# Kernel tuning notes

Hardware: AMD Instinct MI355X
Metric: run time of the kernel (lower is better)

Reference implementation:

```python
import jax, jax.numpy as jnp
import numpy as np

D_MODEL = 512
N_PAIRS = D_MODEL // 2
B, T = 8, 4096


def setup_inputs() -> dict:
    key = jax.random.key(0)
    ks = jax.random.split(key, 7)
    scale = 1.0 / np.sqrt(D_MODEL)
    return {
        "x_seq": jax.random.normal(ks[0], (B, T, D_MODEL), dtype=jnp.float32),
        "W_angle": jax.random.uniform(ks[1], (D_MODEL, N_PAIRS), jnp.float32, -scale, scale),
        "b_angle": jnp.zeros((N_PAIRS,), jnp.float32),
        "W_decay": jax.random.uniform(ks[2], (D_MODEL, 1), jnp.float32, -scale, scale),
        "b_decay": jnp.full((1,), 1.4, jnp.float32),
        "W_input": jax.random.uniform(ks[3], (D_MODEL, D_MODEL), jnp.float32, -scale, scale),
        "b_input": jax.random.uniform(ks[4], (D_MODEL,), jnp.float32, -scale, scale),
    }


def _givens_ssm(x_seq, W_angle, b_angle, W_decay, b_decay, W_input, b_input):
    Bb, Tt, D = x_seq.shape
    P = D // 2
    angles = jnp.einsum("btd,dp->btp", x_seq, W_angle) + b_angle          # [B,T,P]
    decays = jax.nn.sigmoid(jnp.einsum("btd,dk->btk", x_seq, W_decay) + b_decay)[..., 0]  # [B,T]
    inj = jnp.einsum("btd,de->bte", x_seq, W_input) + b_input              # [B,T,D]
    inj = inj.reshape(Bb, Tt, P, 2)

    # scan over time: h_t = decay_t * Rot(angles_t) h_{t-1} + inj_t, pairwise 2x2 rotations
    def step(h, inp):
        a, d, u = inp  # a:[B,P], d:[B], u:[B,P,2]
        c, s = jnp.cos(a), jnp.sin(a)
        he = c * h[..., 0] - s * h[..., 1]
        ho = s * h[..., 0] + c * h[..., 1]
        h_new = d[:, None, None] * jnp.stack([he, ho], axis=-1) + u
        return h_new, h_new

    h0 = jnp.zeros((Bb, P, 2), x_seq.dtype)
    xs = (jnp.swapaxes(angles, 0, 1), jnp.swapaxes(decays, 0, 1), jnp.swapaxes(inj, 0, 1))
    _, states = jax.lax.scan(step, h0, xs)  # [T,B,P,2]
    return jnp.swapaxes(states, 0, 1).reshape(Bb, Tt, D)


def reference(x_seq, W_angle, b_angle, W_decay, b_decay, W_input, b_input):
    return _givens_ssm(x_seq, W_angle, b_angle, W_decay, b_decay, W_input, b_input)
```

## Files before the change

### kernel.cpp

```cpp
#include <hip/hip_runtime.h>
#include <math.h>

typedef _Float16 half_t;
typedef __attribute__((ext_vector_type(8))) _Float16 half8;
typedef __attribute__((ext_vector_type(4))) _Float16 half4;
typedef __attribute__((ext_vector_type(2))) _Float16 half2v;
typedef __attribute__((ext_vector_type(4))) float floatx4;

#define BATCH   8
#define SEQ     4096
#define DM      512
#define NP      256
#define M_TOT   32768
#define NTOT    768
#define CHUNKS  512
#define CHUNK_LEN 8

__device__ __forceinline__ void async_load16(const void* g, void* l) {
    __builtin_amdgcn_global_load_lds((const __attribute__((address_space(1))) void*)g,
                                     (__attribute__((address_space(3))) void*)l,
                                     16, 0, 0);
}

__global__ __launch_bounds__(256) void decay_convert(const float* __restrict__ X,
                                                     const float* __restrict__ Wd,
                                                     const float* __restrict__ bd,
                                                     float* __restrict__ dec,
                                                     half_t* __restrict__ Xh) {
    const int wave = threadIdx.x >> 6;
    const int lane = threadIdx.x & 63;
    const int row0 = blockIdx.x * 8 + wave * 2;
    const float4* x0 = (const float4*)(X + (size_t)row0 * DM);
    const float4* x1 = x0 + 128;
    const float4* wd = (const float4*)Wd;
    float4 a0 = x0[2 * lane], a1 = x0[2 * lane + 1];
    float4 b0 = x1[2 * lane], b1 = x1[2 * lane + 1];
    float4 w0 = wd[2 * lane], w1 = wd[2 * lane + 1];
    float s0 = a0.x * w0.x + a0.y * w0.y + a0.z * w0.z + a0.w * w0.w
             + a1.x * w1.x + a1.y * w1.y + a1.z * w1.z + a1.w * w1.w;
    float s1 = b0.x * w0.x + b0.y * w0.y + b0.z * w0.z + b0.w * w0.w
             + b1.x * w1.x + b1.y * w1.y + b1.z * w1.z + b1.w * w1.w;
    half8 h0 = {(half_t)a0.x, (half_t)a0.y, (half_t)a0.z, (half_t)a0.w,
                (half_t)a1.x, (half_t)a1.y, (half_t)a1.z, (half_t)a1.w};
    half8 h1 = {(half_t)b0.x, (half_t)b0.y, (half_t)b0.z, (half_t)b0.w,
                (half_t)b1.x, (half_t)b1.y, (half_t)b1.z, (half_t)b1.w};
    *(half8*)(Xh + (size_t)row0 * DM + lane * 8) = h0;
    *(half8*)(Xh + (size_t)(row0 + 1) * DM + lane * 8) = h1;
#pragma unroll
    for (int off = 32; off > 0; off >>= 1) {
        s0 += __shfl_down(s0, off, 64);
        s1 += __shfl_down(s1, off, 64);
    }
    if (lane == 0) {
        dec[row0]     = 1.0f / (1.0f + __expf(-(s0 + bd[0])));
        dec[row0 + 1] = 1.0f / (1.0f + __expf(-(s1 + bd[0])));
    }
}

__global__ __launch_bounds__(256) void wcat_transpose(const float* __restrict__ Wi,
                                                      const float* __restrict__ Wa,
                                                      half_t* __restrict__ Wt) {
    const int idx = blockIdx.x * 256 + threadIdx.x;
    const int n = idx >> 9;
    const int k = idx & 511;
    float v = (n < DM) ? Wi[(size_t)k * DM + n] : Wa[(size_t)k * NP + (n - DM)];
    Wt[idx] = (half_t)v;
}

__global__ __launch_bounds__(256) void gemm_fused(const half_t* __restrict__ Xh,
                                                  const half_t* __restrict__ Wt,
                                                  const float* __restrict__ bi,
                                                  const float* __restrict__ ba,
                                                  half_t* __restrict__ inj,
                                                  half_t* __restrict__ angles) {
    __shared__ __align__(16) char As[8192];
    __shared__ __align__(16) char Bs[8192];

    const int bm   = blockIdx.x;
    const int bn   = blockIdx.y;
    const int tid  = threadIdx.x;
    const int wave = tid >> 6;
    const int lane = tid & 63;
    const int quad = lane >> 4;
    const int l16  = lane & 15;
    const int wrow = wave >> 1;
    const int wcol = wave & 1;

    floatx4 acc[4][4];
#pragma unroll
    for (int i = 0; i < 4; ++i)
#pragma unroll
        for (int j = 0; j < 4; ++j) acc[i][j] = (floatx4){0.f, 0.f, 0.f, 0.f};

    const int s0 = wave * 128 + lane;
    const int s1 = s0 + 64;
    const int r0 = s0 >> 2, kql0 = (s0 & 3) ^ ((r0 >> 1) & 3);
    const int r1 = s1 >> 2, kql1 = (s1 & 3) ^ ((r1 >> 1) & 3);
    const half_t* gA0 = Xh + (size_t)(bm * 128 + r0) * DM + kql0 * 8;
    const half_t* gA1 = Xh + (size_t)(bm * 128 + r1) * DM + kql1 * 8;
    const half_t* gB0 = Wt + (size_t)(bn * 128 + r0) * DM + kql0 * 8;
    const half_t* gB1 = Wt + (size_t)(bn * 128 + r1) * DM + kql1 * 8;
    char* lA0 = As + wave * 2048;
    char* lA1 = As + wave * 2048 + 1024;
    char* lB0 = Bs + wave * 2048;
    char* lB1 = Bs + wave * 2048 + 1024;

    for (int k0 = 0; k0 < DM; k0 += 32) {
        async_load16(gA0 + k0, lA0);
        async_load16(gA1 + k0, lA1);
        async_load16(gB0 + k0, lB0);
        async_load16(gB1 + k0, lB1);
        __syncthreads();

        half8 af[4], bf[4];
#pragma unroll
        for (int mt = 0; mt < 4; ++mt) {
            const int r = wrow * 64 + mt * 16 + l16;
            af[mt] = *(const half8*)(As + r * 64 + ((quad ^ ((r >> 1) & 3)) << 4));
        }
#pragma unroll
        for (int nt = 0; nt < 4; ++nt) {
            const int r = wcol * 64 + nt * 16 + l16;
            bf[nt] = *(const half8*)(Bs + r * 64 + ((quad ^ ((r >> 1) & 3)) << 4));
        }
#pragma unroll
        for (int mt = 0; mt < 4; ++mt)
#pragma unroll
            for (int nt = 0; nt < 4; ++nt)
                acc[mt][nt] = __builtin_amdgcn_mfma_f32_16x16x32_f16(af[mt], bf[nt],
                                                                     acc[mt][nt], 0, 0, 0);
        __syncthreads();
    }

    const bool  is_inj = (bn < 4);
    half_t*     dst    = is_inj ? inj    : angles;
    const int   ldd    = is_inj ? DM     : NP;
    const int   cb     = is_inj ? bn * 128 : bn * 128 - DM;

    float bias[4];
#pragma unroll
    for (int nt = 0; nt < 4; ++nt) {
        const int colt = wcol * 64 + nt * 16 + l16;
        bias[nt] = is_inj ? bi[bn * 128 + colt] : ba[bn * 128 + colt - DM];
    }

    half_t* Cs = (half_t*)As;
#pragma unroll
    for (int rh = 0; rh < 2; ++rh) {
        __syncthreads();
        if (wrow == rh) {
#pragma unroll
            for (int mt = 0; mt < 4; ++mt)
#pragma unroll
                for (int nt = 0; nt < 4; ++nt)
#pragma unroll
                    for (int r = 0; r < 4; ++r) {
                        const int lr = mt * 16 + quad * 4 + r;
                        const int lc = wcol * 64 + nt * 16 + l16;
                        Cs[lr * 128 + (lc ^ (((lr >> 2) & 3) << 4))] =
                            (half_t)(acc[mt][nt][r] + bias[nt]);
                    }
        }
        __syncthreads();
#pragma unroll
        for (int it = 0; it < 4; ++it) {
            const int idx = it * 256 + tid;
            const int rr  = idx >> 4;
            const int cc  = (idx & 15) * 8;
            const int grow = bm * 128 + rh * 64 + rr;
            half8 v = *(half8*)(Cs + rr * 128 + (cc ^ (((rr >> 2) & 3) << 4)));
            *(half8*)(dst + (size_t)grow * ldd + cb + cc) = v;
        }
    }
}

__global__ __launch_bounds__(256) void scan_sum1(const half_t* __restrict__ angles,
                                                 const float* __restrict__ decays,
                                                 const half_t* __restrict__ inj,
                                                 float* __restrict__ thetaC,
                                                 float4* __restrict__ hend,
                                                 float* __restrict__ Dprod) {
    const int b   = blockIdx.x >> 8;
    const int sub = threadIdx.x >> 7;
    const int th  = threadIdx.x & 127;
    const int c   = (blockIdx.x & 255) * 2 + sub;
    const int p0  = th * 2;
    const int t0  = c * CHUNK_LEN;

    const half_t* ap = angles + (size_t)(b * SEQ + t0) * NP + p0;
    const half4*  up = (const half4*)(inj + (size_t)(b * SEQ + t0) * DM) + th;
    const float*  dp = decays + b * SEQ + t0;

    half2v a[8]; half4 u[8]; float d[8];
#pragma unroll
    for (int j = 0; j < 8; ++j) {
        a[j] = *(const half2v*)(ap + (size_t)j * NP);
        u[j] = up[(size_t)j * 128];
        d[j] = dp[j];
    }

    float h0a = 0, h1a = 0, h0b = 0, h1b = 0, tha = 0, thb = 0, dc = 1.0f;
#pragma unroll
    for (int j = 0; j < 8; ++j) {
        float a0 = (float)a[j][0], a1 = (float)a[j][1];
        float dd = d[j];
        float s0, c0, s1, c1;
        __sincosf(a0, &s0, &c0);
        __sincosf(a1, &s1, &c1);
        float n0a = fmaf(dd, c0 * h0a - s0 * h1a, (float)u[j][0]);
        float n1a = fmaf(dd, s0 * h0a + c0 * h1a, (float)u[j][1]);
        float n0b = fmaf(dd, c1 * h0b - s1 * h1b, (float)u[j][2]);
        float n1b = fmaf(dd, s1 * h0b + c1 * h1b, (float)u[j][3]);
        h0a = n0a; h1a = n1a; h0b = n0b; h1b = n1b;
        tha += a0; thb += a1; dc *= dd;
    }
    const size_t cbase = (size_t)(b * CHUNKS + c) * NP + p0;
    *(float2*)(thetaC + cbase) = make_float2(tha, thb);
    hend[cbase >> 1] = make_float4(h0a, h1a, h0b, h1b);
    if (th == 0) Dprod[b * CHUNKS + c] = dc;
}

__global__ __launch_bounds__(512) void scan_chunks(const float* __restrict__ thetaC,
                                                   const float4* __restrict__ hend,
                                                   const float* __restrict__ Dprod,
                                                   float4* __restrict__ hentry) {
    const int b  = blockIdx.x >> 7;
    const int pp = blockIdx.x & 127;
    const int c  = threadIdx.x;

    __shared__ float  sTa[512], sTb[512], sD[512];
    __shared__ float4 sV[512];

    const size_t idx = (size_t)(b * CHUNKS + c);
    const float2 th2 = *(const float2*)(thetaC + idx * NP + pp * 2);
    float4 v = hend[idx * 128 + pp];
    float  D = Dprod[idx];
    float tha = th2.x, thb = th2.y;

    sTa[c] = tha; sTb[c] = thb; sD[c] = D; sV[c] = v;

#pragma unroll
    for (int o = 1; o < 512; o <<= 1) {
        __syncthreads();
        float lta = 0.f, ltb = 0.f, lD = 0.f;
        float4 lv = make_float4(0.f, 0.f, 0.f, 0.f);
        const bool has = (c >= o);
        if (has) { lta = sTa[c - o]; ltb = sTb[c - o]; lD = sD[c - o]; lv = sV[c - o]; }
        __syncthreads();
        if (has) {
            float s0, c0, s1, c1;
            __sincosf(tha, &s0, &c0);
            __sincosf(thb, &s1, &c1);
            v.x = fmaf(D, c0 * lv.x - s0 * lv.y, v.x);
            v.y = fmaf(D, s0 * lv.x + c0 * lv.y, v.y);
            v.z = fmaf(D, c1 * lv.z - s1 * lv.w, v.z);
            v.w = fmaf(D, s1 * lv.z + c1 * lv.w, v.w);
            tha += lta; thb += ltb; D *= lD;
            sTa[c] = tha; sTb[c] = thb; sD[c] = D; sV[c] = v;
        }
    }
    __syncthreads();
    const float4 e = (c == 0) ? make_float4(0.f, 0.f, 0.f, 0.f) : sV[c - 1];
    hentry[idx * 128 + pp] = e;
}

__global__ __launch_bounds__(256) void scan_final(const half_t* __restrict__ angles,
                                                  const float* __restrict__ decays,
                                                  const half_t* __restrict__ inj,
                                                  const float4* __restrict__ hentry,
                                                  float* __restrict__ out) {
    const int b   = blockIdx.x >> 8;
    const int sub = threadIdx.x >> 7;
    const int th  = threadIdx.x & 127;
    const int c   = (blockIdx.x & 255) * 2 + sub;
    const int p0  = th * 2;
    const int t0  = c * CHUNK_LEN;

    const half_t* ap = angles + (size_t)(b * SEQ + t0) * NP + p0;
    const half4*  up = (const half4*)(inj + (size_t)(b * SEQ + t0) * DM) + th;
    float4*       op = (float4*)out + (size_t)(b * SEQ + t0) * 128 + (p0 >> 1);
    const float*  dp = decays + b * SEQ + t0;

    float4 v = hentry[(size_t)(b * CHUNKS + c) * 128 + (p0 >> 1)];
    float h0a = v.x, h1a = v.y, h0b = v.z, h1b = v.w;

    half2v a[8]; half4 u[8]; float d[8];
#pragma unroll
    for (int j = 0; j < 8; ++j) {
        a[j] = *(const half2v*)(ap + (size_t)j * NP);
        u[j] = up[(size_t)j * 128];
        d[j] = dp[j];
    }

#pragma unroll
    for (int j = 0; j < 8; ++j) {
        float a0 = (float)a[j][0], a1 = (float)a[j][1];
        float dd = d[j];
        float s0, c0, s1, c1;
        __sincosf(a0, &s0, &c0);
        __sincosf(a1, &s1, &c1);
        float n0a = fmaf(dd, c0 * h0a - s0 * h1a, (float)u[j][0]);
        float n1a = fmaf(dd, s0 * h0a + c0 * h1a, (float)u[j][1]);
        float n0b = fmaf(dd, c1 * h0b - s1 * h1b, (float)u[j][2]);
        float n1b = fmaf(dd, s1 * h0b + c1 * h1b, (float)u[j][3]);
        h0a = n0a; h1a = n1a; h0b = n0b; h1b = n1b;
        op[(size_t)j * 128] = make_float4(h0a, h1a, h0b, h1b);
    }
}

extern "C" void kernel_launch(void* const* d_in, const int* in_sizes, int n_in,
                              void* d_out, int out_size, void* d_ws, size_t ws_size,
                              hipStream_t stream) {
    const float* x  = (const float*)d_in[0];
    const float* Wa = (const float*)d_in[1];
    const float* ba = (const float*)d_in[2];
    const float* Wd = (const float*)d_in[3];
    const float* bd = (const float*)d_in[4];
    const float* Wi = (const float*)d_in[5];
    const float* bi = (const float*)d_in[6];
    float* out = (float*)d_out;

    char* ws = (char*)d_ws;
    half_t* x_h     = (half_t*)(ws);
    float*  thetaC  = (float*)(ws);
    float4* hend    = (float4*)(ws + 4194304);
    float*  Dprod   = (float*)(ws + 12582912);
    float4* hentry  = (float4*)(ws + 12599296);
    half_t* inj_h   = (half_t*)(ws + 33554432);
    half_t* angles  = (half_t*)(ws + 67108864);
    float*  decays  = (float*)(ws + 83886080);
    half_t* Wcat_t  = (half_t*)(ws + 84017152);

    decay_convert<<<M_TOT / 8, 256, 0, stream>>>(x, Wd, bd, decays, x_h);
    wcat_transpose<<<(NTOT * DM) / 256, 256, 0, stream>>>(Wi, Wa, Wcat_t);
    gemm_fused<<<dim3(M_TOT / 128, NTOT / 128), 256, 0, stream>>>(x_h, Wcat_t, bi, ba, inj_h, angles);

    scan_sum1<<<BATCH * CHUNKS / 2, 256, 0, stream>>>(angles, decays, inj_h, thetaC, hend, Dprod);
    scan_chunks<<<BATCH * 128, 512, 0, stream>>>(thetaC, hend, Dprod, hentry);
    scan_final<<<BATCH * CHUNKS / 2, 256, 0, stream>>>(angles, decays, inj_h, hentry, out);
}
```

Baseline: 214.7 us.

## Precompute cos/sin in GEMM epilogue, stage injection in output, double chunk length

The GEMM epilogue now computes sin/cos of the angles once and stores them as two fp16 planes. The injection term is written directly into the fp32 output buffer, and the final scan reads and overwrites it in place. The chunk scan carries composed rotation cos/sin pairs instead of summed angles, and chunk length doubles to 16, which halves the chunk count. This removes the repeated sincos work from both scan passes and the fp16 injection buffer. In exchange the injection is read in fp32 (more bytes), the angle data is stored twice, and the epilogue does more work.

Result: slower. 228.0 us (+6.2%).

```diff
diff --git a/kernel.cpp b/kernel.cpp
--- a/kernel.cpp
+++ b/kernel.cpp
@@ -13,8 +13,8 @@
 #define NP      256
 #define M_TOT   32768
 #define NTOT    768
-#define CHUNKS  512
-#define CHUNK_LEN 8
+#define CHUNKS  256
+#define CHUNK_LEN 16
 
 __device__ __forceinline__ void async_load16(const void* g, void* l) {
     __builtin_amdgcn_global_load_lds((const __attribute__((address_space(1))) void*)g,
@@ -71,8 +71,9 @@
                                                   const half_t* __restrict__ Wt,
                                                   const float* __restrict__ bi,
                                                   const float* __restrict__ ba,
-                                                  half_t* __restrict__ inj,
-                                                  half_t* __restrict__ angles) {
+                                                  float* __restrict__ out,
+                                                  half_t* __restrict__ cosb,
+                                                  half_t* __restrict__ sinb) {
     __shared__ __align__(16) char As[8192];
     __shared__ __align__(16) char Bs[8192];
 
@@ -132,95 +133,119 @@
         __syncthreads();
     }
 
-    const bool  is_inj = (bn < 4);
-    half_t*     dst    = is_inj ? inj    : angles;
-    const int   ldd    = is_inj ? DM     : NP;
-    const int   cb     = is_inj ? bn * 128 : bn * 128 - DM;
-
-    float bias[4];
-#pragma unroll
-    for (int nt = 0; nt < 4; ++nt) {
-        const int colt = wcol * 64 + nt * 16 + l16;
-        bias[nt] = is_inj ? bi[bn * 128 + colt] : ba[bn * 128 + colt - DM];
-    }
-
-    half_t* Cs = (half_t*)As;
-#pragma unroll
-    for (int rh = 0; rh < 2; ++rh) {
-        __syncthreads();
-        if (wrow == rh) {
-#pragma unroll
-            for (int mt = 0; mt < 4; ++mt)
-#pragma unroll
-                for (int nt = 0; nt < 4; ++nt)
-#pragma unroll
-                    for (int r = 0; r < 4; ++r) {
-                        const int lr = mt * 16 + quad * 4 + r;
-                        const int lc = wcol * 64 + nt * 16 + l16;
-                        Cs[lr * 128 + (lc ^ (((lr >> 2) & 3) << 4))] =
-                            (half_t)(acc[mt][nt][r] + bias[nt]);
-                    }
-        }
-        __syncthreads();
-#pragma unroll
-        for (int it = 0; it < 4; ++it) {
-            const int idx = it * 256 + tid;
-            const int rr  = idx >> 4;
-            const int cc  = (idx & 15) * 8;
-            const int grow = bm * 128 + rh * 64 + rr;
-            half8 v = *(half8*)(Cs + rr * 128 + (cc ^ (((rr >> 2) & 3) << 4)));
-            *(half8*)(dst + (size_t)grow * ldd + cb + cc) = v;
-        }
-    }
-}
-
-__global__ __launch_bounds__(256) void scan_sum1(const half_t* __restrict__ angles,
+    const bool is_inj = (bn < 4);
+    if (is_inj) {
+        const int colbase = bn * 128 + wcol * 64;
+#pragma unroll
+        for (int nt = 0; nt < 4; ++nt) {
+            const int col = colbase + nt * 16 + l16;
+            const float bias = bi[col];
+#pragma unroll
+            for (int mt = 0; mt < 4; ++mt) {
+                const int rowb = bm * 128 + wrow * 64 + mt * 16 + quad * 4;
+#pragma unroll
+                for (int r = 0; r < 4; ++r)
+                    out[(size_t)(rowb + r) * DM + col] = acc[mt][nt][r] + bias;
+            }
+        }
+    } else {
+        float bias[4];
+#pragma unroll
+        for (int nt = 0; nt < 4; ++nt) {
+            const int colt = wcol * 64 + nt * 16 + l16;
+            bias[nt] = ba[bn * 128 + colt - DM];
+        }
+        half_t* Cs = (half_t*)As;
+        const int cb = bn * 128 - DM;
+#pragma unroll
+        for (int plane = 0; plane < 2; ++plane) {
+            half_t* pd = plane ? sinb : cosb;
+#pragma unroll
+            for (int rh = 0; rh < 2; ++rh) {
+                __syncthreads();
+                if (wrow == rh) {
+#pragma unroll
+                    for (int mt = 0; mt < 4; ++mt)
+#pragma unroll
+                        for (int nt = 0; nt < 4; ++nt)
+#pragma unroll
+                            for (int r = 0; r < 4; ++r) {
+                                const int lr = mt * 16 + quad * 4 + r;
+                                const int lc = wcol * 64 + nt * 16 + l16;
+                                const float av = acc[mt][nt][r] + bias[nt];
+                                float sv, cv;
+                                __sincosf(av, &sv, &cv);
+                                Cs[lr * 128 + (lc ^ (((lr >> 2) & 3) << 4))] =
+                                    (half_t)(plane ? sv : cv);
+                            }
+                }
+                __syncthreads();
+#pragma unroll
+                for (int it = 0; it < 4; ++it) {
+                    const int idx = it * 256 + tid;
+                    const int rr  = idx >> 4;
+                    const int cc  = (idx & 15) * 8;
+                    const int grow = bm * 128 + rh * 64 + rr;
+                    half8 v = *(half8*)(Cs + rr * 128 + (cc ^ (((rr >> 2) & 3) << 4)));
+                    *(half8*)(pd + (size_t)grow * NP + cb + cc) = v;
+                }
+            }
+        }
+    }
+}
+
+__global__ __launch_bounds__(256) void scan_sum1(const half_t* __restrict__ cosb,
+                                                 const half_t* __restrict__ sinb,
                                                  const float* __restrict__ decays,
-                                                 const half_t* __restrict__ inj,
-                                                 float* __restrict__ thetaC,
+                                                 const float* __restrict__ injf,
+                                                 float4* __restrict__ csC,
                                                  float4* __restrict__ hend,
                                                  float* __restrict__ Dprod) {
-    const int b   = blockIdx.x >> 8;
+    const int b   = blockIdx.x >> 7;
     const int sub = threadIdx.x >> 7;
     const int th  = threadIdx.x & 127;
-    const int c   = (blockIdx.x & 255) * 2 + sub;
+    const int c   = (blockIdx.x & 127) * 2 + sub;
     const int p0  = th * 2;
     const int t0  = c * CHUNK_LEN;
 
-    const half_t* ap = angles + (size_t)(b * SEQ + t0) * NP + p0;
-    const half4*  up = (const half4*)(inj + (size_t)(b * SEQ + t0) * DM) + th;
+    const half_t* cp = cosb + (size_t)(b * SEQ + t0) * NP + p0;
+    const half_t* sp = sinb + (size_t)(b * SEQ + t0) * NP + p0;
+    const float4* up = (const float4*)injf + (size_t)(b * SEQ + t0) * 128 + th;
     const float*  dp = decays + b * SEQ + t0;
 
-    half2v a[8]; half4 u[8]; float d[8];
-#pragma unroll
-    for (int j = 0; j < 8; ++j) {
-        a[j] = *(const half2v*)(ap + (size_t)j * NP);
-        u[j] = up[(size_t)j * 128];
-        d[j] = dp[j];
-    }
-
-    float h0a = 0, h1a = 0, h0b = 0, h1b = 0, tha = 0, thb = 0, dc = 1.0f;
-#pragma unroll
-    for (int j = 0; j < 8; ++j) {
-        float a0 = (float)a[j][0], a1 = (float)a[j][1];
-        float dd = d[j];
-        float s0, c0, s1, c1;
-        __sincosf(a0, &s0, &c0);
-        __sincosf(a1, &s1, &c1);
-        float n0a = fmaf(dd, c0 * h0a - s0 * h1a, (float)u[j][0]);
-        float n1a = fmaf(dd, s0 * h0a + c0 * h1a, (float)u[j][1]);
-        float n0b = fmaf(dd, c1 * h0b - s1 * h1b, (float)u[j][2]);
-        float n1b = fmaf(dd, s1 * h0b + c1 * h1b, (float)u[j][3]);
+    half2v cb[16], sb[16]; float4 u[16]; float d[16];
+#pragma unroll
+    for (int j = 0; j < 16; ++j) {
+        cb[j] = *(const half2v*)(cp + (size_t)j * NP);
+        sb[j] = *(const half2v*)(sp + (size_t)j * NP);
+        u[j]  = up[(size_t)j * 128];
+        d[j]  = dp[j];
+    }
+
+    float h0a = 0, h1a = 0, h0b = 0, h1b = 0;
+    float CcA = 1.f, SsA = 0.f, CcB = 1.f, SsB = 0.f, dc = 1.f;
+#pragma unroll
+    for (int j = 0; j < 16; ++j) {
+        const float c0 = (float)cb[j][0], c1 = (float)cb[j][1];
+        const float s0 = (float)sb[j][0], s1 = (float)sb[j][1];
+        const float dd = d[j];
+        float n0a = fmaf(dd, c0 * h0a - s0 * h1a, u[j].x);
+        float n1a = fmaf(dd, s0 * h0a + c0 * h1a, u[j].y);
+        float n0b = fmaf(dd, c1 * h0b - s1 * h1b, u[j].z);
+        float n1b = fmaf(dd, s1 * h0b + c1 * h1b, u[j].w);
         h0a = n0a; h1a = n1a; h0b = n0b; h1b = n1b;
-        tha += a0; thb += a1; dc *= dd;
-    }
-    const size_t cbase = (size_t)(b * CHUNKS + c) * NP + p0;
-    *(float2*)(thetaC + cbase) = make_float2(tha, thb);
-    hend[cbase >> 1] = make_float4(h0a, h1a, h0b, h1b);
+        float tCA = c0 * CcA - s0 * SsA, tSA = s0 * CcA + c0 * SsA;
+        float tCB = c1 * CcB - s1 * SsB, tSB = s1 * CcB + c1 * SsB;
+        CcA = tCA; SsA = tSA; CcB = tCB; SsB = tSB;
+        dc *= dd;
+    }
+    const size_t idx = (size_t)(b * CHUNKS + c) * 128 + th;
+    csC[idx]  = make_float4(CcA, SsA, CcB, SsB);
+    hend[idx] = make_float4(h0a, h1a, h0b, h1b);
     if (th == 0) Dprod[b * CHUNKS + c] = dc;
 }
 
-__global__ __launch_bounds__(512) void scan_chunks(const float* __restrict__ thetaC,
+__global__ __launch_bounds__(256) void scan_chunks(const float4* __restrict__ csC,
                                                    const float4* __restrict__ hend,
                                                    const float* __restrict__ Dprod,
                                                    float4* __restrict__ hentry) {
@@ -228,81 +253,81 @@
     const int pp = blockIdx.x & 127;
     const int c  = threadIdx.x;
 
-    __shared__ float  sTa[512], sTb[512], sD[512];
-    __shared__ float4 sV[512];
-
-    const size_t idx = (size_t)(b * CHUNKS + c);
-    const float2 th2 = *(const float2*)(thetaC + idx * NP + pp * 2);
-    float4 v = hend[idx * 128 + pp];
-    float  D = Dprod[idx];
-    float tha = th2.x, thb = th2.y;
-
-    sTa[c] = tha; sTb[c] = thb; sD[c] = D; sV[c] = v;
-
-#pragma unroll
-    for (int o = 1; o < 512; o <<= 1) {
+    __shared__ float4 sCS[256];
+    __shared__ float4 sV[256];
+    __shared__ float  sD[256];
+
+    const size_t idx = (size_t)(b * CHUNKS + c) * 128 + pp;
+    float4 cs = csC[idx];
+    float4 v  = hend[idx];
+    float  D  = Dprod[b * CHUNKS + c];
+    sCS[c] = cs; sV[c] = v; sD[c] = D;
+
+#pragma unroll
+    for (int o = 1; o < 256; o <<= 1) {
         __syncthreads();
-        float lta = 0.f, ltb = 0.f, lD = 0.f;
-        float4 lv = make_float4(0.f, 0.f, 0.f, 0.f);
+        float4 lcs = make_float4(1.f, 0.f, 1.f, 0.f);
+        float4 lv  = make_float4(0.f, 0.f, 0.f, 0.f);
+        float  lD  = 0.f;
         const bool has = (c >= o);
-        if (has) { lta = sTa[c - o]; ltb = sTb[c - o]; lD = sD[c - o]; lv = sV[c - o]; }
+        if (has) { lcs = sCS[c - o]; lv = sV[c - o]; lD = sD[c - o]; }
         __syncthreads();
         if (has) {
-            float s0, c0, s1, c1;
-            __sincosf(tha, &s0, &c0);
-            __sincosf(thb, &s1, &c1);
-            v.x = fmaf(D, c0 * lv.x - s0 * lv.y, v.x);
-            v.y = fmaf(D, s0 * lv.x + c0 * lv.y, v.y);
-            v.z = fmaf(D, c1 * lv.z - s1 * lv.w, v.z);
-            v.w = fmaf(D, s1 * lv.z + c1 * lv.w, v.w);
-            tha += lta; thb += ltb; D *= lD;
-            sTa[c] = tha; sTb[c] = thb; sD[c] = D; sV[c] = v;
+            v.x = fmaf(D, cs.x * lv.x - cs.y * lv.y, v.x);
+            v.y = fmaf(D, cs.y * lv.x + cs.x * lv.y, v.y);
+            v.z = fmaf(D, cs.z * lv.z - cs.w * lv.w, v.z);
+            v.w = fmaf(D, cs.w * lv.z + cs.z * lv.w, v.w);
+            float nx = cs.x * lcs.x - cs.y * lcs.y;
+            float ny = cs.y * lcs.x + cs.x * lcs.y;
+            float nz = cs.z * lcs.z - cs.w * lcs.w;
+            float nw = cs.w * lcs.z + cs.z * lcs.w;
+            cs = make_float4(nx, ny, nz, nw);
+            D *= lD;
+            sCS[c] = cs; sV[c] = v; sD[c] = D;
         }
     }
     __syncthreads();
-    const float4 e = (c == 0) ? make_float4(0.f, 0.f, 0.f, 0.f) : sV[c - 1];
-    hentry[idx * 128 + pp] = e;
-}
-
-__global__ __launch_bounds__(256) void scan_final(const half_t* __restrict__ angles,
+    hentry[idx] = (c == 0) ? make_float4(0.f, 0.f, 0.f, 0.f) : sV[c - 1];
+}
+
+__global__ __launch_bounds__(256) void scan_final(const half_t* __restrict__ cosb,
+                                                  const half_t* __restrict__ sinb,
                                                   const float* __restrict__ decays,
-                                                  const half_t* __restrict__ inj,
                                                   const float4* __restrict__ hentry,
                                                   float* __restrict__ out) {
-    const int b   = blockIdx.x >> 8;
+    const int b   = blockIdx.x >> 7;
     const int sub = threadIdx.x >> 7;
     const int th  = threadIdx.x & 127;
-    const int c   = (blockIdx.x & 255) * 2 + sub;
+    const int c   = (blockIdx.x & 127) * 2 + sub;
     const int p0  = th * 2;
     const int t0  = c * CHUNK_LEN;
 
-    const half_t* ap = angles + (size_t)(b * SEQ + t0) * NP + p0;
-    const half4*  up = (const half4*)(inj + (size_t)(b * SEQ + t0) * DM) + th;
-    float4*       op = (float4*)out + (size_t)(b * SEQ + t0) * 128 + (p0 >> 1);
+    const half_t* cp = cosb + (size_t)(b * SEQ + t0) * NP + p0;
+    const half_t* sp = sinb + (size_t)(b * SEQ + t0) * NP + p0;
+    float4*       op = (float4*)out + (size_t)(b * SEQ + t0) * 128 + th;
     const float*  dp = decays + b * SEQ + t0;
 
-    float4 v = hentry[(size_t)(b * CHUNKS + c) * 128 + (p0 >> 1)];
+    float4 v = hentry[(size_t)(b * CHUNKS + c) * 128 + th];
     float h0a = v.x, h1a = v.y, h0b = v.z, h1b = v.w;
 
-    half2v a[8]; half4 u[8]; float d[8];
-#pragma unroll
-    for (int j = 0; j < 8; ++j) {
-        a[j] = *(const half2v*)(ap + (size_t)j * NP);
-        u[j] = up[(size_t)j * 128];
-        d[j] = dp[j];
-    }
-
-#pragma unroll
-    for (int j = 0; j < 8; ++j) {
-        float a0 = (float)a[j][0], a1 = (float)a[j][1];
-        float dd = d[j];
-        float s0, c0, s1, c1;
-        __sincosf(a0, &s0, &c0);
-        __sincosf(a1, &s1, &c1);
-        float n0a = fmaf(dd, c0 * h0a - s0 * h1a, (float)u[j][0]);
-        float n1a = fmaf(dd, s0 * h0a + c0 * h1a, (float)u[j][1]);
-        float n0b = fmaf(dd, c1 * h0b - s1 * h1b, (float)u[j][2]);
-        float n1b = fmaf(dd, s1 * h0b + c1 * h1b, (float)u[j][3]);
+    half2v cb[16], sb[16]; float4 u[16]; float d[16];
+#pragma unroll
+    for (int j = 0; j < 16; ++j) {
+        cb[j] = *(const half2v*)(cp + (size_t)j * NP);
+        sb[j] = *(const half2v*)(sp + (size_t)j * NP);
+        u[j]  = op[(size_t)j * 128];
+        d[j]  = dp[j];
+    }
+
+#pragma unroll
+    for (int j = 0; j < 16; ++j) {
+        const float c0 = (float)cb[j][0], c1 = (float)cb[j][1];
+        const float s0 = (float)sb[j][0], s1 = (float)sb[j][1];
+        const float dd = d[j];
+        float n0a = fmaf(dd, c0 * h0a - s0 * h1a, u[j].x);
+        float n1a = fmaf(dd, s0 * h0a + c0 * h1a, u[j].y);
+        float n0b = fmaf(dd, c1 * h0b - s1 * h1b, u[j].z);
+        float n1b = fmaf(dd, s1 * h0b + c1 * h1b, u[j].w);
         h0a = n0a; h1a = n1a; h0b = n0b; h1b = n1b;
         op[(size_t)j * 128] = make_float4(h0a, h1a, h0b, h1b);
     }
@@ -322,20 +347,22 @@
 
     char* ws = (char*)d_ws;
     half_t* x_h     = (half_t*)(ws);
-    float*  thetaC  = (float*)(ws);
+    float4* csC     = (float4*)(ws);
     float4* hend    = (float4*)(ws + 4194304);
-    float*  Dprod   = (float*)(ws + 12582912);
-    float4* hentry  = (float4*)(ws + 12599296);
-    half_t* inj_h   = (half_t*)(ws + 33554432);
-    half_t* angles  = (half_t*)(ws + 67108864);
-    float*  decays  = (float*)(ws + 83886080);
-    half_t* Wcat_t  = (half_t*)(ws + 84017152);
+    float*  Dprod   = (float*)(ws + 8388608);
+    float4* hentry  = (float4*)(ws + 8396800);
+    half_t* cosb    = (half_t*)(ws + 33554432);
+    half_t* sinb    = (half_t*)(ws + 50331648);
+    float*  decays  = (float*)(ws + 67108864);
+    half_t* Wcat_t  = (half_t*)(ws + 67239936);
 
     decay_convert<<<M_TOT / 8, 256, 0, stream>>>(x, Wd, bd, decays, x_h);
     wcat_transpose<<<(NTOT * DM) / 256, 256, 0, stream>>>(Wi, Wa, Wcat_t);
-    gemm_fused<<<dim3(M_TOT / 128, NTOT / 128), 256, 0, stream>>>(x_h, Wcat_t, bi, ba, inj_h, angles);
-
-    scan_sum1<<<BATCH * CHUNKS / 2, 256, 0, stream>>>(angles, decays, inj_h, thetaC, hend, Dprod);
-    scan_chunks<<<BATCH * 128, 512, 0, stream>>>(thetaC, hend, Dprod, hentry);
-    scan_final<<<BATCH * CHUNKS / 2, 256, 0, stream>>>(angles, decays, inj_h, hentry, out);
-}
+    gemm_fused<<<dim3(M_TOT / 128, NTOT / 128), 256, 0, stream>>>(x_h, Wcat_t, bi, ba,
+                                                                  out, cosb, sinb);
+
+    scan_sum1<<<BATCH * CHUNKS / 2, 256, 0, stream>>>(cosb, sinb, decays, out,
+                                                      csC, hend, Dprod);
+    scan_chunks<<<BATCH * 128, 256, 0, stream>>>(csC, hend, Dprod, hentry);
+    scan_final<<<BATCH * CHUNKS / 2, 256, 0, stream>>>(cosb, sinb, decays, hentry, out);
+}
```
